# Optimization experiments

Measured on AMD Instinct MI355X. Metric: run time of the kernel, lower is better.

## Reference

```python
import jax, jax.numpy as jnp
import numpy as np

C, H_IMG = 1, 1024
N_PATCH = 64
L = 12          # blocks
NH = 12         # heads
D = 768         # hidden_d
DH = D // NH    # head dim
MLP = 4 * D
OUT_D = 1000
BATCH = 256
PATCH = H_IMG // N_PATCH
IN_D = C * PATCH
SEQ = N_PATCH + 1


def _pos_emb(pos, dim):
    # faithful to original: exponent uses i directly (2*i/dim), sin for even i, cos for odd i
    p = np.arange(pos, dtype=np.float64)[:, None]
    i = np.arange(dim, dtype=np.float64)[None, :]
    ang = p / np.power(10000.0, 2.0 * i / dim)
    pe = np.where((np.arange(dim)[None, :] % 2) == 0, np.sin(ang), np.cos(ang))
    return jnp.asarray(pe, dtype=jnp.float32)


def setup_inputs() -> dict:
    key = jax.random.key(0)
    ks = jax.random.split(key, 24)
    s = lambda fan: 1.0 / np.sqrt(fan)
    inp = {
        "images": jax.random.normal(ks[0], (BATCH, C, H_IMG), jnp.float32),
        "linear_w": jax.random.uniform(ks[1], (D, IN_D), jnp.float32, -s(IN_D), s(IN_D)),
        "linear_b": jax.random.uniform(ks[2], (D,), jnp.float32, -s(IN_D), s(IN_D)),
        "class_token": jax.random.uniform(ks[3], (1, D), jnp.float32),
        "pos_emb": _pos_emb(SEQ, D),
        "ln1_g": jnp.ones((L, D), jnp.float32),
        "ln1_b": jnp.zeros((L, D), jnp.float32),
        "wq": jax.random.uniform(ks[4], (L, NH, DH, DH), jnp.float32, -s(DH), s(DH)),
        "bq": jax.random.uniform(ks[5], (L, NH, DH), jnp.float32, -s(DH), s(DH)),
        "wk": jax.random.uniform(ks[6], (L, NH, DH, DH), jnp.float32, -s(DH), s(DH)),
        "bk": jax.random.uniform(ks[7], (L, NH, DH), jnp.float32, -s(DH), s(DH)),
        "wv": jax.random.uniform(ks[8], (L, NH, DH, DH), jnp.float32, -s(DH), s(DH)),
        "bv": jax.random.uniform(ks[9], (L, NH, DH), jnp.float32, -s(DH), s(DH)),
        "ln2_g": jnp.ones((L, D), jnp.float32),
        "ln2_b": jnp.zeros((L, D), jnp.float32),
        "w1": jax.random.uniform(ks[10], (L, MLP, D), jnp.float32, -s(D), s(D)),
        "b1": jax.random.uniform(ks[11], (L, MLP), jnp.float32, -s(D), s(D)),
        "w2": jax.random.uniform(ks[12], (L, D, MLP), jnp.float32, -s(MLP), s(MLP)),
        "b2": jax.random.uniform(ks[13], (L, D), jnp.float32, -s(MLP), s(MLP)),
        "head_w": jax.random.uniform(ks[14], (OUT_D, D), jnp.float32, -s(D), s(D)),
        "head_b": jax.random.uniform(ks[15], (OUT_D,), jnp.float32, -s(D), s(D)),
    }
    return inp


def _ln(x, g, b):
    m = jnp.mean(x, axis=-1, keepdims=True)
    v = jnp.var(x, axis=-1, keepdims=True)
    return (x - m) / jnp.sqrt(v + 1e-5) * g + b


def _block(x, g1, be1, wq, bq, wk, bk, wv, bv, g2, be2, w1, bb1, w2, bb2):
    B, S, _ = x.shape
    h = _ln(x, g1, be1).reshape(B, S, NH, DH)  # split heads along feature dim
    q = jnp.einsum('bshd,hed->bshe', h, wq) + bq
    k = jnp.einsum('bshd,hed->bshe', h, wk) + bk
    v = jnp.einsum('bshd,hed->bshe', h, wv) + bv
    scores = jnp.einsum('bshe,bthe->bhst', q, k) / np.sqrt(DH).astype(np.float32)
    attn = jax.nn.softmax(scores, axis=-1)
    o = jnp.einsum('bhst,bthe->bshe', attn, v).reshape(B, S, D)
    x = x + o
    h2 = _ln(x, g2, be2)
    m = jax.nn.gelu(jnp.einsum('bsd,fd->bsf', h2, w1) + bb1, approximate=False)
    m = jnp.einsum('bsf,df->bsd', m, w2) + bb2
    return x + m


def reference(images, linear_w, linear_b, class_token, pos_emb,
              ln1_g, ln1_b, wq, bq, wk, bk, wv, bv, ln2_g, ln2_b,
              w1, b1, w2, b2, head_w, head_b):
    n = images.shape[0]
    # patchify: [n, c, h] -> [n, n_patch, c*patch_size] (flatten is (c, patch) row-major)
    patches = images.reshape(n, C, N_PATCH, PATCH).transpose(0, 2, 1, 3).reshape(n, N_PATCH, IN_D)
    tokens = jnp.einsum('npi,di->npd', patches, linear_w) + linear_b
    cls = jnp.broadcast_to(class_token[None], (n, 1, D))
    x = jnp.concatenate([cls, tokens], axis=1) + pos_emb[None]
    for l in range(L):
        x = _block(x, ln1_g[l], ln1_b[l], wq[l], bq[l], wk[l], bk[l], wv[l], bv[l],
                   ln2_g[l], ln2_b[l], w1[l], b1[l], w2[l], b2[l])
    cls_out = x[:, 0]
    logits = cls_out @ head_w.T + head_b
    return jax.nn.softmax(logits, axis=-1)
```

## Files before the change

kernel.cpp:

```cpp
#include <hip/hip_runtime.h>

#define NLAYER 12
#define NHEAD  12
#define DHEAD  64
#define DMODEL 768
#define SEQL   65
#define NBATCH 256
#define MTOK   (NBATCH*SEQL)
#define MLPD   3072

typedef _Float16 f16;
typedef f16  f16x8 __attribute__((ext_vector_type(8)));
typedef f16  f16x4 __attribute__((ext_vector_type(4)));
typedef float f32x4 __attribute__((ext_vector_type(4)));

#define MFMA(a,b,c) __builtin_amdgcn_mfma_f32_16x16x32_f16(a,b,c,0,0,0)

__device__ __forceinline__ void gload16(const void* g, void* l) {
  __builtin_amdgcn_global_load_lds((const __attribute__((address_space(1))) void*)g,
                                   (__attribute__((address_space(3))) void*)l, 16, 0, 0);
}

__device__ __forceinline__ float gelu_f(float v) {
  float z = fabsf(v) * 0.70710678118654752f;
  float t = 1.f / (1.f + 0.3275911f * z);
  float p = ((((1.061405429f*t - 1.453152027f)*t + 1.421413741f)*t
              - 0.284496736f)*t + 0.254829592f)*t;
  float erfz = 1.f - p * __expf(-z*z);
  float erfv = copysignf(erfz, v);
  return 0.5f * v * (1.f + erfv);
}

__global__ __launch_bounds__(256) void cvt_f16k(const float* __restrict__ in,
                                                f16* __restrict__ out, int n) {
  long i = ((long)blockIdx.x*256 + threadIdx.x)*4;
  if (i >= n) return;
  const float4 v = *(const float4*)(in + i);
  f16x4 o = { (f16)v.x, (f16)v.y, (f16)v.z, (f16)v.w };
  *(f16x4*)(out + i) = o;
}

__global__ __launch_bounds__(256) void patch_embed(
    const float* __restrict__ images, const float* __restrict__ lw,
    const float* __restrict__ lb, const float* __restrict__ cls,
    const float* __restrict__ pe, float* __restrict__ x) {
  const int s = blockIdx.x, n = blockIdx.y, tid = threadIdx.x;
  __shared__ float p[16];
  if (s > 0 && tid < 16) p[tid] = images[(long)n*1024 + (s-1)*16 + tid];
  __syncthreads();
  float* xr = x + ((long)n*SEQL + s)*DMODEL;
  #pragma unroll
  for (int j = 0; j < 3; ++j) {
    int d = tid + j*256;
    float v;
    if (s == 0) {
      v = cls[d] + pe[d];
    } else {
      float acc = lb[d];
      #pragma unroll
      for (int i = 0; i < 16; ++i) acc += p[i]*lw[d*16+i];
      v = acc + pe[s*DMODEL + d];
    }
    xr[d] = v;
  }
}

__global__ __launch_bounds__(256) void ln_kernel(
    const float* __restrict__ x, const float* __restrict__ g,
    const float* __restrict__ b, f16* __restrict__ out) {
  const int tid = threadIdx.x, wave = tid >> 6, lane = tid & 63;
  #pragma unroll
  for (int rr = 0; rr < 2; ++rr) {
    const long row = (long)blockIdx.x*8 + wave*2 + rr;
    const float* xr = x + row*DMODEL;
    float4 v[3];
    #pragma unroll
    for (int j = 0; j < 3; ++j) v[j] = *(const float4*)(xr + lane*4 + j*256);
    float s = 0.f, s2 = 0.f;
    #pragma unroll
    for (int j = 0; j < 3; ++j) {
      s  += v[j].x + v[j].y + v[j].z + v[j].w;
      s2 += v[j].x*v[j].x + v[j].y*v[j].y + v[j].z*v[j].z + v[j].w*v[j].w;
    }
    #pragma unroll
    for (int o = 32; o >= 1; o >>= 1) { s += __shfl_xor(s, o); s2 += __shfl_xor(s2, o); }
    float mean = s * (1.f/768.f);
    float var  = s2 * (1.f/768.f) - mean*mean;
    float rstd = rsqrtf(var + 1e-5f);
    f16* orow = out + row*DMODEL;
    #pragma unroll
    for (int j = 0; j < 3; ++j) {
      const float4 gv = *(const float4*)(g + lane*4 + j*256);
      const float4 bv = *(const float4*)(b + lane*4 + j*256);
      f16x4 o4 = { (f16)((v[j].x-mean)*rstd*gv.x + bv.x),
                   (f16)((v[j].y-mean)*rstd*gv.y + bv.y),
                   (f16)((v[j].z-mean)*rstd*gv.z + bv.z),
                   (f16)((v[j].w-mean)*rstd*gv.w + bv.w) };
      *(f16x4*)(orow + lane*4 + j*256) = o4;
    }
  }
}

__global__ __launch_bounds__(320) void attn_kernel(
    const f16* __restrict__ h, const f16* __restrict__ wq, const f16* __restrict__ wk,
    const f16* __restrict__ wv, const float* __restrict__ bq, const float* __restrict__ bk,
    const float* __restrict__ bv, float* __restrict__ x) {
  __shared__ __align__(16) f16 HsPs[80*104];
  __shared__ __align__(16) f16 Qs[80*72];
  __shared__ __align__(16) f16 Ks[80*72];
  __shared__ __align__(16) f16 Vt[64*104];
  const int hd = blockIdx.x, b = blockIdx.y;
  const int tid = threadIdx.x, wave = tid>>6, lane = tid&63;
  const int lc = lane & 15, lg = lane >> 4;
  const f16* hbase = h + ((long)b*SEQL)*DMODEL + hd*DHEAD;

  for (int c = tid; c < 80*8; c += 320) {
    int s = c >> 3, ec = (c & 7)*8;
    uint4 val = {0u,0u,0u,0u};
    if (s < SEQL) val = *(const uint4*)(hbase + (long)s*DMODEL + ec);
    *(uint4*)&HsPs[s*104 + ec] = val;
  }
  for (int c = tid; c < 64*104/8; c += 320) {
    uint4 z = {0u,0u,0u,0u};
    *(uint4*)&Vt[c*8] = z;
  }
  __syncthreads();

  for (int task = wave; task < 15; task += 5) {
    int mat = task / 5, mt = task % 5;
    const f16* W = (mat == 0 ? wq : mat == 1 ? wk : wv) + hd*DHEAD*DHEAD;
    const float* bias = (mat == 0 ? bq : mat == 1 ? bk : bv) + hd*DHEAD;
    #pragma unroll
    for (int nt = 0; nt < 4; ++nt) {
      f32x4 a = {0.f,0.f,0.f,0.f};
      #pragma unroll
      for (int kt = 0; kt < 2; ++kt) {
        f16x8 af = *(const f16x8*)&HsPs[(mt*16 + lc)*104 + kt*32 + lg*8];
        f16x8 bf = *(const f16x8*)&W[(nt*16 + lc)*DHEAD + kt*32 + lg*8];
        a = MFMA(af, bf, a);
      }
      float bb = bias[nt*16 + lc];
      #pragma unroll
      for (int r = 0; r < 4; ++r) {
        int s = mt*16 + lg*4 + r;
        int e = nt*16 + lc;
        float v = a[r] + bb;
        if (mat == 0)      Qs[s*72 + e] = (f16)v;
        else if (mat == 1) Ks[s*72 + e] = (f16)v;
        else               Vt[e*104 + s] = (f16)v;
      }
    }
  }
  __syncthreads();

  for (int mt = wave; mt < 5; mt += 5) {
    {
      uint2 z = {0u,0u};
      *(uint2*)&HsPs[(mt*16 + (lane>>2))*104 + 80 + (lane&3)*4] = z;
    }
    f32x4 sc[5];
    #pragma unroll
    for (int nt = 0; nt < 5; ++nt) {
      f32x4 a = {0.f,0.f,0.f,0.f};
      #pragma unroll
      for (int kt = 0; kt < 2; ++kt) {
        f16x8 af = *(const f16x8*)&Qs[(mt*16 + lc)*72 + kt*32 + lg*8];
        f16x8 bf = *(const f16x8*)&Ks[(nt*16 + lc)*72 + kt*32 + lg*8];
        a = MFMA(af, bf, a);
      }
      sc[nt] = a;
    }
    #pragma unroll
    for (int r = 0; r < 4; ++r) {
      float vals[5];
      #pragma unroll
      for (int nt = 0; nt < 5; ++nt) {
        float v = sc[nt][r]*0.125f;
        if (nt*16 + lc > 64) v = -1e30f;
        vals[nt] = v;
      }
      float mx = vals[0];
      #pragma unroll
      for (int nt = 1; nt < 5; ++nt) mx = fmaxf(mx, vals[nt]);
      #pragma unroll
      for (int o = 8; o >= 1; o >>= 1) mx = fmaxf(mx, __shfl_xor(mx, o, 16));
      float sum = 0.f, p[5];
      #pragma unroll
      for (int nt = 0; nt < 5; ++nt) { p[nt] = __expf(vals[nt]-mx); sum += p[nt]; }
      #pragma unroll
      for (int o = 8; o >= 1; o >>= 1) sum += __shfl_xor(sum, o, 16);
      float inv = 1.f/sum;
      int row = mt*16 + lg*4 + r;
      #pragma unroll
      for (int nt = 0; nt < 5; ++nt) HsPs[row*104 + nt*16 + lc] = (f16)(p[nt]*inv);
    }
    f32x4 oacc[4];
    #pragma unroll
    for (int nt = 0; nt < 4; ++nt) {
      f32x4 a = {0.f,0.f,0.f,0.f};
      #pragma unroll
      for (int kt = 0; kt < 3; ++kt) {
        f16x8 af = *(const f16x8*)&HsPs[(mt*16 + lc)*104 + kt*32 + lg*8];
        f16x8 bf = *(const f16x8*)&Vt[(nt*16 + lc)*104 + kt*32 + lg*8];
        a = MFMA(af, bf, a);
      }
      oacc[nt] = a;
    }
    float* xb = x + ((long)b*SEQL)*DMODEL + hd*DHEAD;
    #pragma unroll
    for (int nt = 0; nt < 4; ++nt) {
      #pragma unroll
      for (int r = 0; r < 4; ++r) {
        int s = mt*16 + lg*4 + r;
        if (s < SEQL) {
          int e = nt*16 + lc;
          xb[(long)s*DMODEL + e] += oacc[nt][r];
        }
      }
    }
  }
}

template<int ACT>
__global__ __launch_bounds__(512) void gemm256(
    const f16* __restrict__ A, const f16* __restrict__ B,
    const float* __restrict__ bias, void* __restrict__ Cout,
    int M, int N, int K) {
  __shared__ __align__(16) f16 lds[49152];
  const int tid = threadIdx.x;
  const int wid = tid >> 6, lane = tid & 63;
  const int lr = lane & 15, lg4 = lane >> 4;
  const int wr = wid >> 2, wc = wid & 3;

  const int gx = gridDim.x;
  const int nwg = gx * gridDim.y;
  const int orig = blockIdx.y * gx + blockIdx.x;
  const int q8 = nwg >> 3, r8 = nwg & 7;
  const int xcd = orig & 7, lin = orig >> 3;
  const int wgid = (xcd < r8 ? xcd*(q8+1) : r8*(q8+1) + (xcd - r8)*q8) + lin;
  const int bx = wgid % gx, by = wgid / gx;

  const long m0 = (long)by * 256, n0 = (long)bx * 256;

  f32x4 acc[8][4];
  #pragma unroll
  for (int i = 0; i < 8; ++i)
    #pragma unroll
    for (int j = 0; j < 4; ++j) acc[i][j] = (f32x4){0.f,0.f,0.f,0.f};

  const int NT = K >> 5;
  const long offA0 = (long)((tid >> 6)*16 + (lane & 15))*K + (lane >> 4)*8;
  const long offA1 = offA0 + 128*(long)K;
  const f16* Abase = A + m0*K;
  const f16* Bbase = B + n0*K;

  auto stage = [&](int t) {
    f16* da = &lds[(t % 3)*16384];
    f16* db = da + 8192;
    const f16* Ap = Abase + t*32;
    const f16* Bp = Bbase + t*32;
    gload16(Ap + offA0, &da[tid*8]);
    gload16(Ap + offA1, &da[(tid+512)*8]);
    gload16(Bp + offA0, &db[tid*8]);
    gload16(Bp + offA1, &db[(tid+512)*8]);
  };

  stage(0); stage(1);

  for (int t = 0; t < NT; ++t) {
    const f16* As = &lds[(t % 3)*16384];
    const f16* Bs = As + 8192;
    if (t + 1 < NT) asm volatile("s_waitcnt vmcnt(4) lgkmcnt(0)" ::: "memory");
    else            asm volatile("s_waitcnt vmcnt(0) lgkmcnt(0)" ::: "memory");
    asm volatile("s_barrier" ::: "memory");
    if (t + 2 < NT) stage(t + 2);
    f16x8 af[8], bf[4];
    #pragma unroll
    for (int mf = 0; mf < 8; ++mf)
      af[mf] = *(const f16x8*)&As[(wr*8 + mf)*512 + lane*8];
    #pragma unroll
    for (int nf = 0; nf < 4; ++nf)
      bf[nf] = *(const f16x8*)&Bs[(wc*4 + nf)*512 + lane*8];
    __builtin_amdgcn_s_setprio(1);
    #pragma unroll
    for (int mf = 0; mf < 8; ++mf)
      #pragma unroll
      for (int nf = 0; nf < 4; ++nf)
        acc[mf][nf] = MFMA(af[mf], bf[nf], acc[mf][nf]);
    __builtin_amdgcn_s_setprio(0);
  }

  __syncthreads();

  if (ACT == 0) {
    f16* Cf = (f16*)Cout;
    char* Ct = (char*)lds;
    #pragma unroll
    for (int H = 0; H < 2; ++H) {
      #pragma unroll
      for (int nf = 0; nf < 4; ++nf) {
        int col = wc*64 + nf*16 + lr;
        float bv = bias[(int)n0 + col];
        #pragma unroll
        for (int mh = 0; mh < 4; ++mh) {
          #pragma unroll
          for (int r2 = 0; r2 < 4; ++r2) {
            int rloc = wr*64 + mh*16 + lg4*4 + r2;
            int byte = rloc*512 + ((col*2) ^ ((rloc & 15) << 4));
            *(f16*)(Ct + byte) = (f16)gelu_f(acc[H*4 + mh][nf][r2] + bv);
          }
        }
      }
      __syncthreads();
      #pragma unroll
      for (int i = 0; i < 8; ++i) {
        int g = i*512 + tid;
        int rloc = g >> 5, ch = g & 31;
        int byte = rloc*512 + ((ch ^ (rloc & 15)) << 4);
        f16x8 val = *(const f16x8*)(Ct + byte);
        long grow = m0 + (rloc >> 6)*128 + H*64 + (rloc & 63);
        *(f16x8*)(Cf + grow*(long)N + n0 + ch*8) = val;
      }
      __syncthreads();
    }
  } else {
    float* Cf = (float*)Cout;
    #pragma unroll
    for (int nf = 0; nf < 4; ++nf) {
      int col = (int)n0 + wc*64 + nf*16 + lr;
      float bv = bias[col];
      #pragma unroll
      for (int mf = 0; mf < 8; ++mf) {
        #pragma unroll
        for (int r2 = 0; r2 < 4; ++r2) {
          long row = m0 + wr*128 + mf*16 + lg4*4 + r2;
          Cf[row*(long)N + col] += acc[mf][nf][r2] + bv;
        }
      }
    }
  }
}

__global__ __launch_bounds__(256) void head_kernel(
    const float* __restrict__ x, const float* __restrict__ hw,
    const float* __restrict__ hb, float* __restrict__ out) {
  const int b = blockIdx.x, tid = threadIdx.x;
  __shared__ float cls[768];
  __shared__ float red[8];
  const float* xr = x + (long)b*SEQL*DMODEL;
  #pragma unroll
  for (int j = 0; j < 3; ++j) cls[tid + j*256] = xr[tid + j*256];
  __syncthreads();
  float lgv[4];
  #pragma unroll
  for (int j = 0; j < 4; ++j) {
    int c = tid + j*256;
    float acc = -1e30f;
    if (c < 1000) {
      const float* wr = hw + (long)c*768;
      float s_ = 0.f;
      for (int i = 0; i < 768; ++i) s_ += cls[i]*wr[i];
      acc = s_ + hb[c];
    }
    lgv[j] = acc;
  }
  const int wave = tid>>6, lane = tid&63;
  float mx = fmaxf(fmaxf(lgv[0],lgv[1]),fmaxf(lgv[2],lgv[3]));
  #pragma unroll
  for (int o = 32; o >= 1; o >>= 1) mx = fmaxf(mx, __shfl_xor(mx, o));
  if (lane == 0) red[wave] = mx;
  __syncthreads();
  mx = fmaxf(fmaxf(red[0],red[1]),fmaxf(red[2],red[3]));
  float e[4]; float sum = 0.f;
  #pragma unroll
  for (int j = 0; j < 4; ++j) {
    int c = tid + j*256;
    e[j] = (c < 1000) ? expf(lgv[j]-mx) : 0.f;
    sum += e[j];
  }
  #pragma unroll
  for (int o = 32; o >= 1; o >>= 1) sum += __shfl_xor(sum, o);
  if (lane == 0) red[4+wave] = sum;
  __syncthreads();
  sum = red[4]+red[5]+red[6]+red[7];
  float inv = 1.f/sum;
  #pragma unroll
  for (int j = 0; j < 4; ++j) {
    int c = tid + j*256;
    if (c < 1000) out[(long)b*1000 + c] = e[j]*inv;
  }
}

extern "C" void kernel_launch(void* const* d_in, const int* in_sizes, int n_in,
                              void* d_out, int out_size, void* d_ws, size_t ws_size,
                              hipStream_t stream) {
  const float* images     = (const float*)d_in[0];
  const float* linear_w   = (const float*)d_in[1];
  const float* linear_b   = (const float*)d_in[2];
  const float* class_tok  = (const float*)d_in[3];
  const float* pos_emb    = (const float*)d_in[4];
  const float* ln1_g      = (const float*)d_in[5];
  const float* ln1_b      = (const float*)d_in[6];
  const float* wq         = (const float*)d_in[7];
  const float* bq         = (const float*)d_in[8];
  const float* wk         = (const float*)d_in[9];
  const float* bk         = (const float*)d_in[10];
  const float* wv         = (const float*)d_in[11];
  const float* bv         = (const float*)d_in[12];
  const float* ln2_g      = (const float*)d_in[13];
  const float* ln2_b      = (const float*)d_in[14];
  const float* w1         = (const float*)d_in[15];
  const float* b1         = (const float*)d_in[16];
  const float* w2         = (const float*)d_in[17];
  const float* b2         = (const float*)d_in[18];
  const float* head_w     = (const float*)d_in[19];
  const float* head_b     = (const float*)d_in[20];

  char* ws = (char*)d_ws;
  float* xbuf = (float*)(ws + 0);
  f16*   hbuf = (f16*)(ws + 51118080);
  f16*   mbuf = (f16*)(ws + 76677120);
  f16*   w1all = (f16*)(ws + 178913280);
  f16*   w2all = (f16*)(ws + 235536384);
  f16*   wqbB  = (f16*)(ws + 292159488);
  f16*   wkbB  = (f16*)(ws + 293339136);
  f16*   wvbB  = (f16*)(ws + 294518784);
  f16*   w1b  = (f16*)(ws + 178913280);
  f16*   w2b  = (f16*)(ws + 183631872);
  f16*   wqbS = (f16*)(ws + 188350464);
  f16*   wkbS = (f16*)(ws + 189530112);
  f16*   wvbS = (f16*)(ws + 190709760);
  if (ws_size < 191889408ull) return;
  const bool big = ws_size >= 295698432ull;
  f16* wqb = big ? wqbB : wqbS;
  f16* wkb = big ? wkbB : wkbS;
  f16* wvb = big ? wvbB : wvbS;

  patch_embed<<<dim3(SEQL, NBATCH), 256, 0, stream>>>(images, linear_w, linear_b,
                                                      class_tok, pos_emb, xbuf);
  cvt_f16k<<<576, 256, 0, stream>>>(wq, wqb, 589824);
  cvt_f16k<<<576, 256, 0, stream>>>(wk, wkb, 589824);
  cvt_f16k<<<576, 256, 0, stream>>>(wv, wvb, 589824);
  if (big) {
    cvt_f16k<<<27648, 256, 0, stream>>>(w1, w1all, 28311552);
    cvt_f16k<<<27648, 256, 0, stream>>>(w2, w2all, 28311552);
  }

  for (int l = 0; l < NLAYER; ++l) {
    ln_kernel<<<MTOK/8, 256, 0, stream>>>(xbuf, ln1_g + l*768, ln1_b + l*768, hbuf);
    attn_kernel<<<dim3(NHEAD, NBATCH), 320, 0, stream>>>(
        hbuf, wqb + l*49152, wkb + l*49152, wvb + l*49152,
        bq + l*768, bk + l*768, bv + l*768, xbuf);
    ln_kernel<<<MTOK/8, 256, 0, stream>>>(xbuf, ln2_g + l*768, ln2_b + l*768, hbuf);
    f16* w1p = big ? (w1all + (long)l*2359296) : w1b;
    f16* w2p = big ? (w2all + (long)l*2359296) : w2b;
    if (!big) cvt_f16k<<<2304, 256, 0, stream>>>(w1 + (long)l*2359296, w1b, 2359296);
    gemm256<0><<<dim3(MLPD/256, MTOK/256), 512, 0, stream>>>(
        hbuf, w1p, b1 + l*3072, (void*)mbuf, MTOK, MLPD, DMODEL);
    if (!big) cvt_f16k<<<2304, 256, 0, stream>>>(w2 + (long)l*2359296, w2b, 2359296);
    gemm256<1><<<dim3(DMODEL/256, MTOK/256), 512, 0, stream>>>(
        mbuf, w2p, b2 + l*768, (void*)xbuf, MTOK, DMODEL, MLPD);
  }
  head_kernel<<<NBATCH, 256, 0, stream>>>(xbuf, head_w, head_b, (float*)d_out);
}
```

Baseline: 5.226 ms.

## Shrink MLP GEMM tiles to 128x128 and split-K the down projection

Replaces the 256x256 tile, 512-thread GEMM with a 128x128 tile, 256-thread kernel sized for three blocks per CU. The down projection (N=768) gets a two-way split over K, with results combined into the residual by atomicAdd and the bias added only by the first split. The goal is better CU occupancy and load balance, since the old down-projection grid had few blocks. The cost is less data reuse per tile, extra atomic traffic on the fp32 residual, and a sum order that is no longer deterministic.

Measured after the change: 5.951 ms. +13.9%, slower.

```diff
diff --git a/kernel.cpp b/kernel.cpp
--- a/kernel.cpp
+++ b/kernel.cpp
@@ -222,15 +222,15 @@
 }
 
 template<int ACT>
-__global__ __launch_bounds__(512) void gemm256(
+__global__ __launch_bounds__(256, 3) void gemm128(
     const f16* __restrict__ A, const f16* __restrict__ B,
     const float* __restrict__ bias, void* __restrict__ Cout,
-    int M, int N, int K) {
-  __shared__ __align__(16) f16 lds[49152];
+    int M, int N, int Kext, int LDK) {
+  __shared__ __align__(16) f16 lds[24576];
   const int tid = threadIdx.x;
-  const int wid = tid >> 6, lane = tid & 63;
+  const int wave = tid >> 6, lane = tid & 63;
   const int lr = lane & 15, lg4 = lane >> 4;
-  const int wr = wid >> 2, wc = wid & 3;
+  const int wm = (wave >> 1) * 64, wn = (wave & 1) * 64;
 
   const int gx = gridDim.x;
   const int nwg = gx * gridDim.y;
@@ -239,51 +239,52 @@
   const int xcd = orig & 7, lin = orig >> 3;
   const int wgid = (xcd < r8 ? xcd*(q8+1) : r8*(q8+1) + (xcd - r8)*q8) + lin;
   const int bx = wgid % gx, by = wgid / gx;
-
-  const long m0 = (long)by * 256, n0 = (long)bx * 256;
-
-  f32x4 acc[8][4];
-  #pragma unroll
-  for (int i = 0; i < 8; ++i)
+  const int kh = blockIdx.z;
+
+  const long m0 = (long)by * 128, n0 = (long)bx * 128;
+
+  f32x4 acc[4][4];
+  #pragma unroll
+  for (int i = 0; i < 4; ++i)
     #pragma unroll
     for (int j = 0; j < 4; ++j) acc[i][j] = (f32x4){0.f,0.f,0.f,0.f};
 
-  const int NT = K >> 5;
-  const long offA0 = (long)((tid >> 6)*16 + (lane & 15))*K + (lane >> 4)*8;
-  const long offA1 = offA0 + 128*(long)K;
-  const f16* Abase = A + m0*K;
-  const f16* Bbase = B + n0*K;
+  const int NT = Kext >> 5;
+  const long off0 = (long)((tid >> 6)*16 + (tid & 15))*LDK + ((tid >> 4) & 3)*8;
+  const long off1 = off0 + 64*(long)LDK;
+  const f16* Abase = A + m0*(long)LDK + (long)kh*Kext;
+  const f16* Bbase = B + n0*(long)LDK + (long)kh*Kext;
 
   auto stage = [&](int t) {
-    f16* da = &lds[(t % 3)*16384];
-    f16* db = da + 8192;
+    f16* da = &lds[(t % 3)*8192];
+    f16* db = da + 4096;
     const f16* Ap = Abase + t*32;
     const f16* Bp = Bbase + t*32;
-    gload16(Ap + offA0, &da[tid*8]);
-    gload16(Ap + offA1, &da[(tid+512)*8]);
-    gload16(Bp + offA0, &db[tid*8]);
-    gload16(Bp + offA1, &db[(tid+512)*8]);
+    gload16(Ap + off0, &da[tid*8]);
+    gload16(Ap + off1, &da[(tid+256)*8]);
+    gload16(Bp + off0, &db[tid*8]);
+    gload16(Bp + off1, &db[(tid+256)*8]);
   };
 
   stage(0); stage(1);
 
   for (int t = 0; t < NT; ++t) {
-    const f16* As = &lds[(t % 3)*16384];
-    const f16* Bs = As + 8192;
+    const f16* As = &lds[(t % 3)*8192];
+    const f16* Bs = As + 4096;
     if (t + 1 < NT) asm volatile("s_waitcnt vmcnt(4) lgkmcnt(0)" ::: "memory");
     else            asm volatile("s_waitcnt vmcnt(0) lgkmcnt(0)" ::: "memory");
     asm volatile("s_barrier" ::: "memory");
     if (t + 2 < NT) stage(t + 2);
-    f16x8 af[8], bf[4];
-    #pragma unroll
-    for (int mf = 0; mf < 8; ++mf)
-      af[mf] = *(const f16x8*)&As[(wr*8 + mf)*512 + lane*8];
+    f16x8 af[4], bf[4];
+    #pragma unroll
+    for (int mf = 0; mf < 4; ++mf)
+      af[mf] = *(const f16x8*)&As[wm*32 + mf*512 + lane*8];
     #pragma unroll
     for (int nf = 0; nf < 4; ++nf)
-      bf[nf] = *(const f16x8*)&Bs[(wc*4 + nf)*512 + lane*8];
+      bf[nf] = *(const f16x8*)&Bs[wn*32 + nf*512 + lane*8];
     __builtin_amdgcn_s_setprio(1);
     #pragma unroll
-    for (int mf = 0; mf < 8; ++mf)
+    for (int mf = 0; mf < 4; ++mf)
       #pragma unroll
       for (int nf = 0; nf < 4; ++nf)
         acc[mf][nf] = MFMA(af[mf], bf[nf], acc[mf][nf]);
@@ -293,48 +294,42 @@
   __syncthreads();
 
   if (ACT == 0) {
+    #pragma unroll
+    for (int nf = 0; nf < 4; ++nf) {
+      int col = wn + nf*16 + lr;
+      float bv = bias[(int)n0 + col];
+      #pragma unroll
+      for (int mf = 0; mf < 4; ++mf) {
+        #pragma unroll
+        for (int r2 = 0; r2 < 4; ++r2) {
+          int row = wm + mf*16 + lg4*4 + r2;
+          int byte = (row*256 + col*2) ^ (((row>>2)&7)<<4);
+          *(f16*)((char*)lds + byte) = (f16)gelu_f(acc[mf][nf][r2] + bv);
+        }
+      }
+    }
+    __syncthreads();
     f16* Cf = (f16*)Cout;
-    char* Ct = (char*)lds;
-    #pragma unroll
-    for (int H = 0; H < 2; ++H) {
-      #pragma unroll
-      for (int nf = 0; nf < 4; ++nf) {
-        int col = wc*64 + nf*16 + lr;
-        float bv = bias[(int)n0 + col];
-        #pragma unroll
-        for (int mh = 0; mh < 4; ++mh) {
-          #pragma unroll
-          for (int r2 = 0; r2 < 4; ++r2) {
-            int rloc = wr*64 + mh*16 + lg4*4 + r2;
-            int byte = rloc*512 + ((col*2) ^ ((rloc & 15) << 4));
-            *(f16*)(Ct + byte) = (f16)gelu_f(acc[H*4 + mh][nf][r2] + bv);
-          }
-        }
-      }
-      __syncthreads();
-      #pragma unroll
-      for (int i = 0; i < 8; ++i) {
-        int g = i*512 + tid;
-        int rloc = g >> 5, ch = g & 31;
-        int byte = rloc*512 + ((ch ^ (rloc & 15)) << 4);
-        f16x8 val = *(const f16x8*)(Ct + byte);
-        long grow = m0 + (rloc >> 6)*128 + H*64 + (rloc & 63);
-        *(f16x8*)(Cf + grow*(long)N + n0 + ch*8) = val;
-      }
-      __syncthreads();
+    #pragma unroll
+    for (int i = 0; i < 8; ++i) {
+      int g = i*256 + tid;
+      int row = g >> 4, ch = g & 15;
+      int byte = (row*256 + ch*16) ^ (((row>>2)&7)<<4);
+      f16x8 val = *(const f16x8*)((const char*)lds + byte);
+      *(f16x8*)(Cf + (m0 + row)*(long)N + n0 + ch*8) = val;
     }
   } else {
     float* Cf = (float*)Cout;
     #pragma unroll
     for (int nf = 0; nf < 4; ++nf) {
-      int col = (int)n0 + wc*64 + nf*16 + lr;
-      float bv = bias[col];
-      #pragma unroll
-      for (int mf = 0; mf < 8; ++mf) {
+      int col = (int)n0 + wn + nf*16 + lr;
+      float bv = (kh == 0) ? bias[col] : 0.f;
+      #pragma unroll
+      for (int mf = 0; mf < 4; ++mf) {
         #pragma unroll
         for (int r2 = 0; r2 < 4; ++r2) {
-          long row = m0 + wr*128 + mf*16 + lg4*4 + r2;
-          Cf[row*(long)N + col] += acc[mf][nf][r2] + bv;
+          long row = m0 + wm + mf*16 + lg4*4 + r2;
+          atomicAdd(&Cf[row*(long)N + col], acc[mf][nf][r2] + bv);
         }
       }
     }
@@ -455,11 +450,11 @@
     f16* w1p = big ? (w1all + (long)l*2359296) : w1b;
     f16* w2p = big ? (w2all + (long)l*2359296) : w2b;
     if (!big) cvt_f16k<<<2304, 256, 0, stream>>>(w1 + (long)l*2359296, w1b, 2359296);
-    gemm256<0><<<dim3(MLPD/256, MTOK/256), 512, 0, stream>>>(
-        hbuf, w1p, b1 + l*3072, (void*)mbuf, MTOK, MLPD, DMODEL);
+    gemm128<0><<<dim3(MLPD/128, MTOK/128), 256, 0, stream>>>(
+        hbuf, w1p, b1 + l*3072, (void*)mbuf, MTOK, MLPD, 768, 768);
     if (!big) cvt_f16k<<<2304, 256, 0, stream>>>(w2 + (long)l*2359296, w2b, 2359296);
-    gemm256<1><<<dim3(DMODEL/256, MTOK/256), 512, 0, stream>>>(
-        mbuf, w2p, b2 + l*768, (void*)xbuf, MTOK, DMODEL, MLPD);
+    gemm128<1><<<dim3(DMODEL/128, MTOK/128, 2), 256, 0, stream>>>(
+        mbuf, w2p, b2 + l*768, (void*)xbuf, MTOK, DMODEL, 1536, 3072);
   }
   head_kernel<<<NBATCH, 256, 0, stream>>>(xbuf, head_w, head_b, (float*)d_out);
 }
```
